# Kernel optimization log

Hardware: AMD Instinct MI355X
Metric: run time of the kernel (lower is better)

## Reference

```python
import jax, jax.numpy as jnp
import numpy as np
import math

# LLaMA-7B-style int8 attention (torch-int Int8LlamaAttention)
B, S, HID, NH, HD = 2, 1024, 4096, 32, 128
THETA = 10000.0
# per-tensor quantization scales (as produced by from_float)
S_IN, S_W, S_B = 0.02, 0.01, 0.1
S_Q, S_K, S_V, S_O = 0.05, 0.05, 0.05, 0.05


def _rope_tables(position_ids):
    inv_freq = 1.0 / (THETA ** (jnp.arange(0, HD, 2, dtype=jnp.float32) / HD))
    freqs = position_ids.astype(jnp.float32)[..., None] * inv_freq  # [B,S,HD//2]
    emb = jnp.concatenate([freqs, freqs], axis=-1)  # [B,S,HD]
    return jnp.cos(emb)[:, None], jnp.sin(emb)[:, None]  # [B,1,S,HD]


def _rotate_half(x):
    return jnp.concatenate([-x[..., HD // 2:], x[..., :HD // 2]], axis=-1)


def _quant_i8(x):
    return jnp.clip(jnp.round(x), -128, 127).astype(jnp.int8)


def _w8a8b8o8(x_i8, w_i8, b_i8, alpha, beta):
    # int8 GEMM with int32 accumulation, fused dequant-requant to int8
    acc = jnp.einsum('bsk,nk->bsn', x_i8.astype(jnp.int32), w_i8.astype(jnp.int32))
    return _quant_i8(acc.astype(jnp.float32) * alpha + b_i8.astype(jnp.float32) * beta)


def setup_inputs() -> dict:
    key = jax.random.key(0)
    ks = jax.random.split(key, 9)
    ri8 = lambda k, shp: jax.random.randint(k, shp, -127, 128, dtype=jnp.int8)
    return {
        'hidden_states': jax.random.normal(ks[0], (B, S, HID), jnp.float32),
        'position_ids': jnp.broadcast_to(jnp.arange(S, dtype=jnp.int32), (B, S)),
        'w_q': ri8(ks[1], (HID, HID)),
        'w_k': ri8(ks[2], (HID, HID)),
        'w_v': ri8(ks[3], (HID, HID)),
        'w_o': ri8(ks[4], (HID, HID)),
        'b_q': ri8(ks[5], (HID,)),
        'b_k': ri8(ks[6], (HID,)),
        'b_v': ri8(ks[7], (HID,)),
        'b_o': jax.random.normal(ks[8], (HID,), jnp.float32) * 0.01,
    }


def reference(hidden_states, position_ids, w_q, w_k, w_v, w_o, b_q, b_k, b_v, b_o):
    # quantize activations, run int8 q/k/v projections (W8A8B8O8Linear)
    x_i8 = _quant_i8(hidden_states / S_IN)
    q = _w8a8b8o8(x_i8, w_q, b_q, S_IN * S_W / S_Q, S_B / S_Q)
    k = _w8a8b8o8(x_i8, w_k, b_k, S_IN * S_W / S_K, S_B / S_K)
    v = _w8a8b8o8(x_i8, w_v, b_v, S_IN * S_W / S_V, S_B / S_V)
    to_heads = lambda t: t.reshape(B, S, NH, HD).transpose(0, 2, 1, 3)  # [B,NH,S,HD]
    q, k, v = to_heads(q), to_heads(k), to_heads(v)
    # RoPE applied on dequantized int8 values, requantized for the int8 qk bmm
    cos, sin = _rope_tables(position_ids)
    qf, kf = q.astype(jnp.float32), k.astype(jnp.float32)
    q_i8 = _quant_i8(qf * cos + _rotate_half(qf) * sin)
    k_i8 = _quant_i8(kf * cos + _rotate_half(kf) * sin)
    # BMM_S8T_S8N_F32T: int8 QK^T -> fp32 with scale s_q*s_k, then /sqrt(d)
    attn = jnp.einsum('bhsd,bhtd->bhst', q_i8.astype(jnp.int32), k_i8.astype(jnp.int32))
    attn = attn.astype(jnp.float32) * (S_Q * S_K) / math.sqrt(HD)
    # NOTE: source never applies the attention mask (`attn_weights = attn_weights`)
    p = jax.nn.softmax(attn, axis=-1)
    # probs quantized to int8 with scale 1/127 for BMM_S8T_S8N_S8T
    p_i8 = _quant_i8(p * 127.0)
    ctx = jnp.einsum('bhst,bhtd->bhsd', p_i8.astype(jnp.int32), v.astype(jnp.int32))
    ctx_i8 = _quant_i8(ctx.astype(jnp.float32) * ((1.0 / 127.0) * S_V / S_O))
    ctx_i8 = ctx_i8.transpose(0, 2, 1, 3).reshape(B, S, HID)
    # W8A8BFP32OFP32 o_proj: int8 GEMM, fp32 output + fp32 bias
    out = jnp.einsum('bsk,nk->bsn', ctx_i8.astype(jnp.int32), w_o.astype(jnp.int32))
    return out.astype(jnp.float32) * (S_O * S_W) + b_o
```

## Files before the change

kernel.cpp:

```cpp
#include <hip/hip_runtime.h>
#include <hip/hip_bf16.h>
#include <cstdint>
#include <cstddef>

typedef int v4i __attribute__((ext_vector_type(4)));

#define NH 32
#define HD 128
#define SEQ 1024
#define HID 4096
#define BB 2

__device__ __forceinline__ signed char quant_i8(float x) {
    float r = rintf(x);
    r = fminf(fmaxf(r, -128.0f), 127.0f);
    return (signed char)r;
}

#define GLOAD_LDS16(g, l) \
    __builtin_amdgcn_global_load_lds((const __attribute__((address_space(1))) void*)(g), \
                                     (__attribute__((address_space(3))) void*)(l), 16, 0, 0)

__global__ __launch_bounds__(256) void pack4_i8_kernel(
    const int* __restrict__ s0, const int* __restrict__ s1,
    const int* __restrict__ s2, const int* __restrict__ s3,
    signed char* __restrict__ d0, signed char* __restrict__ d1,
    signed char* __restrict__ d2, signed char* __restrict__ d3, int n4)
{
    int i = blockIdx.x * 256 + threadIdx.x;
    int which = i >> 22;
    int idx = i & ((1 << 22) - 1);
    const int* src = (which == 0) ? s0 : (which == 1) ? s1 : (which == 2) ? s2 : s3;
    signed char* dst = (which == 0) ? d0 : (which == 1) ? d1 : (which == 2) ? d2 : d3;
    int4 v = ((const int4*)src)[idx];
    char4 c;
    c.x = (signed char)v.x; c.y = (signed char)v.y;
    c.z = (signed char)v.z; c.w = (signed char)v.w;
    ((char4*)dst)[idx] = c;
}

__global__ __launch_bounds__(256) void quant_x_kernel(const float* __restrict__ src,
                                                      signed char* __restrict__ dst, int n4) {
    int i = blockIdx.x * 256 + threadIdx.x;
    if (i >= n4) return;
    float4 v = ((const float4*)src)[i];
    char4 c;
    c.x = quant_i8(v.x * 50.0f);
    c.y = quant_i8(v.y * 50.0f);
    c.z = quant_i8(v.z * 50.0f);
    c.w = quant_i8(v.w * 50.0f);
    ((char4*)dst)[i] = c;
}

template<bool F32OUT>
__device__ __forceinline__ void gemm128(
    const signed char* __restrict__ A, const signed char* __restrict__ Bw,
    const void* __restrict__ bias, void* __restrict__ outp,
    int m0, int n0, int N, int K, float alpha, float beta)
{
    __shared__ __align__(16) signed char sA[2][128 * 64];
    __shared__ __align__(16) signed char sB[2][128 * 64];

    const int t    = threadIdx.x;
    const int w    = t >> 6;
    const int lane = t & 63;
    const int lm   = lane & 15;
    const int quad = lane >> 4;
    const int wm   = (w >> 1) * 64;
    const int wn   = (w & 1) * 64;

    int row0 = t >> 2,          cc0 = ((t & 3) - (row0 >> 1)) & 3;
    int row1 = (t + 256) >> 2,  cc1 = (((t + 256) & 3) - (row1 >> 1)) & 3;
    const signed char* aS0 = A  + (size_t)(m0 + row0) * K + cc0 * 16;
    const signed char* aS1 = A  + (size_t)(m0 + row1) * K + cc1 * 16;
    const signed char* bS0 = Bw + (size_t)(n0 + row0) * K + cc0 * 16;
    const signed char* bS1 = Bw + (size_t)(n0 + row1) * K + cc1 * 16;

    v4i acc[4][4] = {};

    GLOAD_LDS16(aS0, &sA[0][t * 16]);
    GLOAD_LDS16(aS1, &sA[0][(t + 256) * 16]);
    GLOAD_LDS16(bS0, &sB[0][t * 16]);
    GLOAD_LDS16(bS1, &sB[0][(t + 256) * 16]);

    const int aslot = ((quad + (wm >> 1) + (lm >> 1)) & 3) << 4;
    const int bslot = ((quad + (wn >> 1) + (lm >> 1)) & 3) << 4;

    int buf = 0;
    for (int k0 = 0; k0 < K; k0 += 64) {
        __syncthreads();
        if (k0 + 64 < K) {
            int nb = buf ^ 1;
            GLOAD_LDS16(aS0 + k0 + 64, &sA[nb][t * 16]);
            GLOAD_LDS16(aS1 + k0 + 64, &sA[nb][(t + 256) * 16]);
            GLOAD_LDS16(bS0 + k0 + 64, &sB[nb][t * 16]);
            GLOAD_LDS16(bS1 + k0 + 64, &sB[nb][(t + 256) * 16]);
        }
        v4i af[4], bf[4];
        #pragma unroll
        for (int i = 0; i < 4; i++)
            af[i] = *(const v4i*)(&sA[buf][(wm + 16 * i + lm) * 64 + aslot]);
        #pragma unroll
        for (int j = 0; j < 4; j++)
            bf[j] = *(const v4i*)(&sB[buf][(wn + 16 * j + lm) * 64 + bslot]);
        __builtin_amdgcn_s_setprio(1);
        #pragma unroll
        for (int i = 0; i < 4; i++)
            #pragma unroll
            for (int j = 0; j < 4; j++)
                acc[i][j] = __builtin_amdgcn_mfma_i32_16x16x64_i8(af[i], bf[j], acc[i][j], 0, 0, 0);
        __builtin_amdgcn_s_setprio(0);
        buf ^= 1;
    }

    const int orow = quad * 4;
    #pragma unroll
    for (int i = 0; i < 4; i++) {
        #pragma unroll
        for (int j = 0; j < 4; j++) {
            #pragma unroll
            for (int r = 0; r < 4; r++) {
                int row = m0 + wm + 16 * i + orow + r;
                int col = n0 + wn + 16 * j + lm;
                float v = (float)acc[i][j][r];
                if (F32OUT) {
                    ((float*)outp)[(size_t)row * N + col] = v * alpha + ((const float*)bias)[col];
                } else {
                    float q = v * alpha + (float)((const int*)bias)[col] * beta;
                    ((signed char*)outp)[(size_t)row * N + col] = quant_i8(q);
                }
            }
        }
    }
}

__global__ __launch_bounds__(256, 4) void gemm_qkv(
    const signed char* __restrict__ x8,
    const signed char* __restrict__ wq, const signed char* __restrict__ wk,
    const signed char* __restrict__ wv,
    const int* __restrict__ bq, const int* __restrict__ bk, const int* __restrict__ bv,
    signed char* __restrict__ q8, signed char* __restrict__ k8, signed char* __restrict__ v8)
{
    const int nblk = blockIdx.x;
    const int which = nblk >> 5;
    const int n0 = (nblk & 31) * 128;
    const int m0 = blockIdx.y * 128;
    const signed char* Bw = (which == 0) ? wq : (which == 1) ? wk : wv;
    const int* bias = (which == 0) ? bq : (which == 1) ? bk : bv;
    signed char* outp = (which == 0) ? q8 : (which == 1) ? k8 : v8;
    gemm128<false>(x8, Bw, bias, outp, m0, n0, HID, HID, 0.004f, 2.0f);
}

__global__ __launch_bounds__(256, 4) void gemm_o(
    const signed char* __restrict__ c8, const signed char* __restrict__ wo,
    const float* __restrict__ bo, float* __restrict__ outp)
{
    gemm128<true>(c8, wo, bo, outp, blockIdx.y * 128, blockIdx.x * 128,
                  HID, HID, 0.0005f, 0.0f);
}

__global__ __launch_bounds__(128) void rope_kernel(
    const int* __restrict__ pos_ids, signed char* __restrict__ q,
    signed char* __restrict__ k, const signed char* __restrict__ v,
    signed char* __restrict__ vt)
{
    const int bid = blockIdx.x;
    const int sg = bid & 127;
    const int h  = (bid >> 7) & (NH - 1);
    const int b  = bid >> 12;
    const int d  = threadIdx.x;
    const int s0 = sg * 8;
    const int bh = b * NH + h;

    float inv = expf(-(float)(2 * (d & 63)) * (9.210340371976184f / 128.0f));

    float qd[8], qp[8], kd[8], kp[8];
    signed char vd[8];
    int pos[8];
    size_t base[8];
    #pragma unroll
    for (int i = 0; i < 8; i++) {
        int s = s0 + i;
        base[i] = ((size_t)(b * SEQ + s) * NH + h) * (size_t)HD;
        pos[i] = pos_ids[b * SEQ + s];
        qd[i] = (float)q[base[i] + d];
        qp[i] = (float)q[base[i] + (d ^ 64)];
        kd[i] = (float)k[base[i] + d];
        kp[i] = (float)k[base[i] + (d ^ 64)];
        vd[i] = v[base[i] + d];
    }
    __syncthreads();

    union { signed char c[8]; int2 i2; } vu;
    #pragma unroll
    for (int i = 0; i < 8; i++) {
        float freq = (float)pos[i] * inv;
        float cs, sn;
        __sincosf(freq, &sn, &cs);
        float rotq = (d < 64) ? -qp[i] : qp[i];
        float rotk = (d < 64) ? -kp[i] : kp[i];
        q[base[i] + d] = quant_i8(qd[i] * cs + rotq * sn);
        k[base[i] + d] = quant_i8(kd[i] * cs + rotk * sn);
        vu.c[i] = vd[i];
    }
    *(int2*)(vt + ((size_t)(bh * HD + d)) * SEQ + s0) = vu.i2;
}

__global__ __launch_bounds__(256) void attn_kernel(
    const signed char* __restrict__ q, const signed char* __restrict__ k,
    const signed char* __restrict__ vt, signed char* __restrict__ ctx)
{
    __shared__ __align__(16) signed char p8[32 * 1040];
    __shared__ float red[128];

    const int w    = threadIdx.x >> 6;
    const int lane = threadIdx.x & 63;
    const int bid  = blockIdx.x;
    const int mt   = bid & 31;
    const int bh   = bid >> 5;
    const int b    = bh >> 5, h = bh & 31;
    const int m0   = mt * 32;
    const int lm   = lane & 15;
    const int quad = lane >> 4;

    const float SCALE = 0.0025f / 11.313708498984761f;
    const float LOG2E = 1.4426950408889634f;

    const signed char* qb_base = q + ((size_t)(b * SEQ + m0 + lm) * NH + h) * (size_t)HD + quad * 16;
    v4i qb0 = *(const v4i*)qb_base;
    v4i qb1 = *(const v4i*)(qb_base + 64);
    const signed char* qb_base2 = qb_base + (size_t)16 * NH * HD;
    v4i qb2 = *(const v4i*)qb_base2;
    v4i qb3 = *(const v4i*)(qb_base2 + 64);

    float vals0[16][4], vals1[16][4];
    #pragma unroll
    for (int j = 0; j < 16; j++) {
        int t0 = w * 256 + j * 16;
        const signed char* kb = k + ((size_t)(b * SEQ + t0 + lm) * NH + h) * (size_t)HD + quad * 16;
        v4i a0 = *(const v4i*)kb;
        v4i a1 = *(const v4i*)(kb + 64);
        v4i acc0 = {}, acc1 = {};
        __builtin_amdgcn_s_setprio(1);
        acc0 = __builtin_amdgcn_mfma_i32_16x16x64_i8(a0, qb0, acc0, 0, 0, 0);
        acc0 = __builtin_amdgcn_mfma_i32_16x16x64_i8(a1, qb1, acc0, 0, 0, 0);
        acc1 = __builtin_amdgcn_mfma_i32_16x16x64_i8(a0, qb2, acc1, 0, 0, 0);
        acc1 = __builtin_amdgcn_mfma_i32_16x16x64_i8(a1, qb3, acc1, 0, 0, 0);
        __builtin_amdgcn_s_setprio(0);
        #pragma unroll
        for (int r = 0; r < 4; r++) {
            vals0[j][r] = (float)acc0[r] * SCALE;
            vals1[j][r] = (float)acc1[r] * SCALE;
        }
    }

    float mx0 = vals0[0][0], mx1 = vals1[0][0];
    #pragma unroll
    for (int j = 0; j < 16; j++)
        #pragma unroll
        for (int r = 0; r < 4; r++) {
            mx0 = fmaxf(mx0, vals0[j][r]);
            mx1 = fmaxf(mx1, vals1[j][r]);
        }
    mx0 = fmaxf(mx0, __shfl_xor(mx0, 16)); mx0 = fmaxf(mx0, __shfl_xor(mx0, 32));
    mx1 = fmaxf(mx1, __shfl_xor(mx1, 16)); mx1 = fmaxf(mx1, __shfl_xor(mx1, 32));
    if (lane < 16) { red[w * 16 + lane] = mx0; red[64 + w * 16 + lane] = mx1; }
    __syncthreads();
    mx0 = fmaxf(fmaxf(red[lm], red[16 + lm]), fmaxf(red[32 + lm], red[48 + lm]));
    mx1 = fmaxf(fmaxf(red[64 + lm], red[80 + lm]), fmaxf(red[96 + lm], red[112 + lm]));

    float sum0 = 0.f, sum1 = 0.f;
    #pragma unroll
    for (int j = 0; j < 16; j++)
        #pragma unroll
        for (int r = 0; r < 4; r++) {
            vals0[j][r] = exp2f((vals0[j][r] - mx0) * LOG2E); sum0 += vals0[j][r];
            vals1[j][r] = exp2f((vals1[j][r] - mx1) * LOG2E); sum1 += vals1[j][r];
        }
    sum0 += __shfl_xor(sum0, 16); sum0 += __shfl_xor(sum0, 32);
    sum1 += __shfl_xor(sum1, 16); sum1 += __shfl_xor(sum1, 32);
    __syncthreads();
    if (lane < 16) { red[w * 16 + lane] = sum0; red[64 + w * 16 + lane] = sum1; }
    __syncthreads();
    sum0 = (red[lm] + red[16 + lm]) + (red[32 + lm] + red[48 + lm]);
    sum1 = (red[64 + lm] + red[80 + lm]) + (red[96 + lm] + red[112 + lm]);
    float sf0 = 127.0f / sum0, sf1 = 127.0f / sum1;

    #pragma unroll
    for (int j = 0; j < 16; j++) {
        union { signed char cc[4]; int ii; } u0, u1;
        #pragma unroll
        for (int r = 0; r < 4; r++) {
            u0.cc[r] = quant_i8(vals0[j][r] * sf0);
            u1.cc[r] = quant_i8(vals1[j][r] * sf1);
        }
        int ch = (((w * 16 + j) + 4 * lm) & 63) * 16 + quad * 4;
        *(int*)(p8 + lm * 1040 + ch) = u0.ii;
        *(int*)(p8 + (16 + lm) * 1040 + ch) = u1.ii;
    }
    __syncthreads();

    v4i accp0[2] = {}, accp1[2] = {};
    for (int kk = 0; kk < SEQ; kk += 64) {
        int ph = (((kk >> 4) + quad) + 4 * lm) & 63;
        v4i af0 = *(const v4i*)(p8 + lm * 1040 + ph * 16);
        v4i af1 = *(const v4i*)(p8 + (16 + lm) * 1040 + ph * 16);
        v4i vb0 = *(const v4i*)(vt + ((size_t)(bh * HD + w * 32 + lm)) * (size_t)SEQ + kk + quad * 16);
        v4i vb1 = *(const v4i*)(vt + ((size_t)(bh * HD + w * 32 + 16 + lm)) * (size_t)SEQ + kk + quad * 16);
        __builtin_amdgcn_s_setprio(1);
        accp0[0] = __builtin_amdgcn_mfma_i32_16x16x64_i8(af0, vb0, accp0[0], 0, 0, 0);
        accp1[0] = __builtin_amdgcn_mfma_i32_16x16x64_i8(af1, vb0, accp1[0], 0, 0, 0);
        accp0[1] = __builtin_amdgcn_mfma_i32_16x16x64_i8(af0, vb1, accp0[1], 0, 0, 0);
        accp1[1] = __builtin_amdgcn_mfma_i32_16x16x64_i8(af1, vb1, accp1[1], 0, 0, 0);
        __builtin_amdgcn_s_setprio(0);
    }
    #pragma unroll
    for (int j = 0; j < 2; j++) {
        #pragma unroll
        for (int r = 0; r < 4; r++) {
            int row = quad * 4 + r;
            int col = w * 32 + j * 16 + lm;
            ctx[((size_t)(b * SEQ + m0 + row) * NH + h) * (size_t)HD + col] =
                quant_i8((float)accp0[j][r] * (1.0f / 127.0f));
            ctx[((size_t)(b * SEQ + m0 + 16 + row) * NH + h) * (size_t)HD + col] =
                quant_i8((float)accp1[j][r] * (1.0f / 127.0f));
        }
    }
}

extern "C" void kernel_launch(void* const* d_in, const int* in_sizes, int n_in,
                              void* d_out, int out_size, void* d_ws, size_t ws_size,
                              hipStream_t stream)
{
    const float* hidden = (const float*)d_in[0];
    const int* pos_ids  = (const int*)d_in[1];
    const int* w_q = (const int*)d_in[2];
    const int* w_k = (const int*)d_in[3];
    const int* w_v = (const int*)d_in[4];
    const int* w_o = (const int*)d_in[5];
    const int* b_q = (const int*)d_in[6];
    const int* b_k = (const int*)d_in[7];
    const int* b_v = (const int*)d_in[8];
    const float* b_o = (const float*)d_in[9];
    float* out = (float*)d_out;

    char* ws = (char*)d_ws;
    const size_t WSZ = (size_t)HID * HID;
    signed char* wq8 = (signed char*)ws;
    signed char* wk8 = wq8 + WSZ;
    signed char* wv8 = wk8 + WSZ;
    signed char* wo8 = wv8 + WSZ;
    signed char* x8  = wo8 + WSZ;
    const size_t ASZ = (size_t)BB * SEQ * HID;
    signed char* q8  = x8 + ASZ;
    signed char* k8  = q8 + ASZ;
    signed char* v8  = k8 + ASZ;
    signed char* vt8 = v8 + ASZ;
    signed char* c8  = vt8 + ASZ;

    int wn4 = HID * HID / 4;
    pack4_i8_kernel<<<4 * wn4 / 256, 256, 0, stream>>>(w_q, w_k, w_v, w_o,
                                                       wq8, wk8, wv8, wo8, wn4);
    int xn4 = (int)(ASZ / 4);
    quant_x_kernel<<<xn4 / 256, 256, 0, stream>>>(hidden, x8, xn4);

    gemm_qkv<<<dim3(96, 16), 256, 0, stream>>>(x8, wq8, wk8, wv8, b_q, b_k, b_v,
                                               q8, k8, v8);

    rope_kernel<<<BB * NH * (SEQ / 8), 128, 0, stream>>>(pos_ids, q8, k8, v8, vt8);
    attn_kernel<<<BB * NH * (SEQ / 32), 256, 0, stream>>>(q8, k8, vt8, c8);

    gemm_o<<<dim3(32, 16), 256, 0, stream>>>(c8, wo8, b_o, out);
}
```

Baseline: 549.0 us.

## Widen GEMM tiles to 128x256 and triple-buffer LDS with register double-buffered fragments

The int8 GEMM helper now computes a 128x256 output tile per block, giving 4x8 MFMA accumulators per wave instead of 4x4. It uses a three-stage LDS ring with explicit vmcnt waits and raw barriers, and ping-pongs fragment registers so LDS reads for the next k-step overlap the current MFMAs. This targets load latency and the LDS traffic per MFMA. The cost is more registers and LDS, so occupancy bounds drop from 4 to 2 and the grids are halved, which leaves fewer blocks in flight.

```diff
diff --git a/kernel.cpp b/kernel.cpp
--- a/kernel.cpp
+++ b/kernel.cpp
@@ -53,71 +53,105 @@
 }
 
 template<bool F32OUT>
-__device__ __forceinline__ void gemm128(
+__device__ __forceinline__ void gemm_pipe(
     const signed char* __restrict__ A, const signed char* __restrict__ Bw,
     const void* __restrict__ bias, void* __restrict__ outp,
     int m0, int n0, int N, int K, float alpha, float beta)
 {
-    __shared__ __align__(16) signed char sA[2][128 * 64];
-    __shared__ __align__(16) signed char sB[2][128 * 64];
+    __shared__ __align__(16) signed char sA[3][128 * 64];
+    __shared__ __align__(16) signed char sB[3][256 * 64];
 
     const int t    = threadIdx.x;
+    const int lane = t & 63;
     const int w    = t >> 6;
-    const int lane = t & 63;
     const int lm   = lane & 15;
     const int quad = lane >> 4;
     const int wm   = (w >> 1) * 64;
-    const int wn   = (w & 1) * 64;
-
-    int row0 = t >> 2,          cc0 = ((t & 3) - (row0 >> 1)) & 3;
-    int row1 = (t + 256) >> 2,  cc1 = (((t + 256) & 3) - (row1 >> 1)) & 3;
-    const signed char* aS0 = A  + (size_t)(m0 + row0) * K + cc0 * 16;
-    const signed char* aS1 = A  + (size_t)(m0 + row1) * K + cc1 * 16;
-    const signed char* bS0 = Bw + (size_t)(n0 + row0) * K + cc0 * 16;
-    const signed char* bS1 = Bw + (size_t)(n0 + row1) * K + cc1 * 16;
-
-    v4i acc[4][4] = {};
-
-    GLOAD_LDS16(aS0, &sA[0][t * 16]);
-    GLOAD_LDS16(aS1, &sA[0][(t + 256) * 16]);
-    GLOAD_LDS16(bS0, &sB[0][t * 16]);
-    GLOAD_LDS16(bS1, &sB[0][(t + 256) * 16]);
-
-    const int aslot = ((quad + (wm >> 1) + (lm >> 1)) & 3) << 4;
-    const int bslot = ((quad + (wn >> 1) + (lm >> 1)) & 3) << 4;
-
-    int buf = 0;
-    for (int k0 = 0; k0 < K; k0 += 64) {
-        __syncthreads();
-        if (k0 + 64 < K) {
-            int nb = buf ^ 1;
-            GLOAD_LDS16(aS0 + k0 + 64, &sA[nb][t * 16]);
-            GLOAD_LDS16(aS1 + k0 + 64, &sA[nb][(t + 256) * 16]);
-            GLOAD_LDS16(bS0 + k0 + 64, &sB[nb][t * 16]);
-            GLOAD_LDS16(bS1 + k0 + 64, &sB[nb][(t + 256) * 16]);
-        }
-        v4i af[4], bf[4];
+    const int wn   = (w & 1) * 128;
+    const int KT   = K >> 6;
+
+    const int ar0 = t >> 2,          ac0 = ((t & 3) - (ar0 >> 1)) & 3;
+    const int ar1 = (t + 256) >> 2,  ac1 = (((t + 256) & 3) - (ar1 >> 1)) & 3;
+    const signed char* aS0 = A + (size_t)(m0 + ar0) * K + ac0 * 16;
+    const signed char* aS1 = A + (size_t)(m0 + ar1) * K + ac1 * 16;
+    const signed char* bS[4];
+    #pragma unroll
+    for (int p = 0; p < 4; p++) {
+        int si = t + 256 * p;
+        int row = si >> 2, c = ((si & 3) - (row >> 1)) & 3;
+        bS[p] = Bw + (size_t)(n0 + row) * K + c * 16;
+    }
+
+    auto stage = [&](int kt) {
+        int s = kt % 3;
+        GLOAD_LDS16(aS0 + kt * 64, &sA[s][t * 16]);
+        GLOAD_LDS16(aS1 + kt * 64, &sA[s][(t + 256) * 16]);
+        #pragma unroll
+        for (int p = 0; p < 4; p++)
+            GLOAD_LDS16(bS[p] + kt * 64, &sB[s][(t + 256 * p) * 16]);
+    };
+
+    const int slot16 = ((quad + (lm >> 1)) & 3) << 4;
+    auto rdfr = [&](int kt, v4i* fr) {
+        const signed char* pA = sA[kt % 3];
+        const signed char* pB = sB[kt % 3];
         #pragma unroll
         for (int i = 0; i < 4; i++)
-            af[i] = *(const v4i*)(&sA[buf][(wm + 16 * i + lm) * 64 + aslot]);
-        #pragma unroll
-        for (int j = 0; j < 4; j++)
-            bf[j] = *(const v4i*)(&sB[buf][(wn + 16 * j + lm) * 64 + bslot]);
-        __builtin_amdgcn_s_setprio(1);
+            fr[i] = *(const v4i*)(pA + (wm + 16 * i + lm) * 64 + slot16);
+        #pragma unroll
+        for (int j = 0; j < 8; j++)
+            fr[4 + j] = *(const v4i*)(pB + (wn + 16 * j + lm) * 64 + slot16);
+    };
+
+    v4i acc[4][8] = {};
+    auto domfma = [&](v4i* fr) {
         #pragma unroll
         for (int i = 0; i < 4; i++)
             #pragma unroll
-            for (int j = 0; j < 4; j++)
-                acc[i][j] = __builtin_amdgcn_mfma_i32_16x16x64_i8(af[i], bf[j], acc[i][j], 0, 0, 0);
-        __builtin_amdgcn_s_setprio(0);
-        buf ^= 1;
+            for (int j = 0; j < 8; j++)
+                acc[i][j] = __builtin_amdgcn_mfma_i32_16x16x64_i8(fr[i], fr[4 + j], acc[i][j], 0, 0, 0);
+    };
+
+    stage(0); stage(1);
+    asm volatile("s_waitcnt vmcnt(6)" ::: "memory");
+    __builtin_amdgcn_s_barrier();
+    v4i fA[12], fB[12];
+    rdfr(0, fA);
+    stage(2);
+    asm volatile("s_waitcnt vmcnt(6)" ::: "memory");
+    __builtin_amdgcn_s_barrier();
+
+    for (int kt = 0; kt < KT; kt += 2) {
+        if (kt + 1 < KT) rdfr(kt + 1, fB);
+        domfma(fA);
+        __builtin_amdgcn_s_barrier();
+        if (kt + 3 < KT) {
+            stage(kt + 3);
+            asm volatile("s_waitcnt vmcnt(6)" ::: "memory");
+        } else {
+            asm volatile("s_waitcnt vmcnt(0)" ::: "memory");
+        }
+        __builtin_amdgcn_s_barrier();
+
+        if (kt + 1 < KT) {
+            if (kt + 2 < KT) rdfr(kt + 2, fA);
+            domfma(fB);
+            __builtin_amdgcn_s_barrier();
+            if (kt + 4 < KT) {
+                stage(kt + 4);
+                asm volatile("s_waitcnt vmcnt(6)" ::: "memory");
+            } else {
+                asm volatile("s_waitcnt vmcnt(0)" ::: "memory");
+            }
+            __builtin_amdgcn_s_barrier();
+        }
     }
 
     const int orow = quad * 4;
     #pragma unroll
     for (int i = 0; i < 4; i++) {
         #pragma unroll
-        for (int j = 0; j < 4; j++) {
+        for (int j = 0; j < 8; j++) {
             #pragma unroll
             for (int r = 0; r < 4; r++) {
                 int row = m0 + wm + 16 * i + orow + r;
@@ -134,29 +168,29 @@
     }
 }
 
-__global__ __launch_bounds__(256, 4) void gemm_qkv(
+__global__ __launch_bounds__(256, 2) void gemm_qkv(
     const signed char* __restrict__ x8,
     const signed char* __restrict__ wq, const signed char* __restrict__ wk,
     const signed char* __restrict__ wv,
     const int* __restrict__ bq, const int* __restrict__ bk, const int* __restrict__ bv,
     signed char* __restrict__ q8, signed char* __restrict__ k8, signed char* __restrict__ v8)
 {
-    const int nblk = blockIdx.x;
-    const int which = nblk >> 5;
-    const int n0 = (nblk & 31) * 128;
+    const int nb = blockIdx.x;
+    const int which = nb >> 4;
+    const int n0 = (nb & 15) * 256;
     const int m0 = blockIdx.y * 128;
     const signed char* Bw = (which == 0) ? wq : (which == 1) ? wk : wv;
     const int* bias = (which == 0) ? bq : (which == 1) ? bk : bv;
     signed char* outp = (which == 0) ? q8 : (which == 1) ? k8 : v8;
-    gemm128<false>(x8, Bw, bias, outp, m0, n0, HID, HID, 0.004f, 2.0f);
-}
-
-__global__ __launch_bounds__(256, 4) void gemm_o(
+    gemm_pipe<false>(x8, Bw, bias, outp, m0, n0, HID, HID, 0.004f, 2.0f);
+}
+
+__global__ __launch_bounds__(256, 2) void gemm_o(
     const signed char* __restrict__ c8, const signed char* __restrict__ wo,
     const float* __restrict__ bo, float* __restrict__ outp)
 {
-    gemm128<true>(c8, wo, bo, outp, blockIdx.y * 128, blockIdx.x * 128,
-                  HID, HID, 0.0005f, 0.0f);
+    gemm_pipe<true>(c8, wo, bo, outp, blockIdx.y * 128, blockIdx.x * 256,
+                    HID, HID, 0.0005f, 0.0f);
 }
 
 __global__ __launch_bounds__(128) void rope_kernel(
@@ -364,11 +398,11 @@
     int xn4 = (int)(ASZ / 4);
     quant_x_kernel<<<xn4 / 256, 256, 0, stream>>>(hidden, x8, xn4);
 
-    gemm_qkv<<<dim3(96, 16), 256, 0, stream>>>(x8, wq8, wk8, wv8, b_q, b_k, b_v,
+    gemm_qkv<<<dim3(48, 16), 256, 0, stream>>>(x8, wq8, wk8, wv8, b_q, b_k, b_v,
                                                q8, k8, v8);
 
     rope_kernel<<<BB * NH * (SEQ / 8), 128, 0, stream>>>(pos_ids, q8, k8, v8, vt8);
     attn_kernel<<<BB * NH * (SEQ / 32), 256, 0, stream>>>(q8, k8, vt8, c8);
 
-    gemm_o<<<dim3(32, 16), 256, 0, stream>>>(c8, wo8, b_o, out);
-}
+    gemm_o<<<dim3(16, 16), 256, 0, stream>>>(c8, wo8, b_o, out);
+}
```

Result: slower. 580.0 us (+5.7%).
